# Kernel tuning notes

Hardware: AMD Instinct MI355X
Metric: run time of the kernel (lower is better)

Reference implementation:

```python
import jax, jax.numpy as jnp
import numpy as np

H = 512      # hidden size
V = 10000    # input_output_size (vocab)
L = 32       # max_length
B = 256      # batch
SOS = 1


def setup_inputs() -> dict:
    key = jax.random.key(0)
    ks = jax.random.split(key, 20)
    g = lambda k, shape: jax.random.normal(k, shape, dtype=jnp.float32) * 0.05
    return dict(
        input_tensor=jax.random.randint(ks[0], (B, L), 0, V),
        target_tensor=jax.random.randint(ks[1], (B, L), 0, V),
        # encoder: embedding + GRU
        enc_embed=g(ks[2], (V, H)),
        enc_w_ih=g(ks[3], (3 * H, H)), enc_w_hh=g(ks[4], (3 * H, H)),
        enc_b_ih=g(ks[5], (3 * H,)), enc_b_hh=g(ks[6], (3 * H,)),
        # attention decoder: embedding + attn + attn_combine + GRU + out
        dec_embed=g(ks[7], (V, H)),
        attn_w=g(ks[8], (L, 2 * H)), attn_b=g(ks[9], (L,)),
        comb_w=g(ks[10], (H, 2 * H)), comb_b=g(ks[11], (H,)),
        dec_w_ih=g(ks[12], (3 * H, H)), dec_w_hh=g(ks[13], (3 * H, H)),
        dec_b_ih=g(ks[14], (3 * H,)), dec_b_hh=g(ks[15], (3 * H,)),
        out_w=g(ks[16], (V, H)), out_b=g(ks[17], (V,)),
    )


def _gru_step(x, h, w_ih, w_hh, b_ih, b_hh):
    # PyTorch GRUCell math. x, h: [B, H]
    gi = x @ w_ih.T + b_ih          # [B, 3H]
    gh = h @ w_hh.T + b_hh          # [B, 3H]
    i_r, i_z, i_n = jnp.split(gi, 3, axis=-1)
    h_r, h_z, h_n = jnp.split(gh, 3, axis=-1)
    r = jax.nn.sigmoid(i_r + h_r)
    z = jax.nn.sigmoid(i_z + h_z)
    n = jnp.tanh(i_n + r * h_n)
    return (1.0 - z) * n + z * h


def reference(input_tensor, target_tensor,
              enc_embed, enc_w_ih, enc_w_hh, enc_b_ih, enc_b_hh,
              dec_embed, attn_w, attn_b, comb_w, comb_b,
              dec_w_ih, dec_w_hh, dec_b_ih, dec_b_hh, out_w, out_b):
    inp_t = input_tensor.T   # [L, B]
    tgt_t = target_tensor.T  # [L, B]
    h0 = jnp.zeros((B, H), dtype=enc_embed.dtype)

    # ---- encoder: scan over time ----
    def enc_step(h, tok):
        x = enc_embed[tok]  # [B, H]
        h2 = _gru_step(x, h, enc_w_ih, enc_w_hh, enc_b_ih, enc_b_hh)
        return h2, h2       # encoder output == hidden

    enc_hidden, enc_outs = jax.lax.scan(enc_step, h0, inp_t)  # enc_outs: [L, B, H]

    # ---- decoder with teacher forcing (phase='train', ratio=1.0) ----
    sos = jnp.full((1, B), SOS, dtype=tgt_t.dtype)
    dec_inputs = jnp.concatenate([sos, tgt_t[:-1]], axis=0)  # [L, B]

    def dec_step(h, tok):
        emb = dec_embed[tok]                                   # [B, H]
        aw = jax.nn.softmax(jnp.concatenate([emb, h], axis=-1) @ attn_w.T + attn_b)  # [B, L]
        applied = jnp.einsum('bl,lbh->bh', aw, enc_outs)       # attention over encoder outputs
        x = jax.nn.relu(jnp.concatenate([emb, applied], axis=-1) @ comb_w.T + comb_b)
        h2 = _gru_step(x, h, dec_w_ih, dec_w_hh, dec_b_ih, dec_b_hh)
        logits = jax.nn.log_softmax(h2 @ out_w.T + out_b)      # [B, V]
        return h2, logits

    _, network_outputs = jax.lax.scan(dec_step, enc_hidden, dec_inputs)  # [L, B, V]
    return network_outputs
```

## Files before the change

kernel.cpp:

```cpp
#include <hip/hip_runtime.h>

#define HD 512
#define VOC 10000
#define SL 32
#define BA 256
#define BH (BA*HD)

typedef __bf16 b16x8 __attribute__((ext_vector_type(8)));
typedef float f32x4 __attribute__((ext_vector_type(4)));
typedef unsigned u32x4 __attribute__((ext_vector_type(4)));

__device__ __forceinline__ ushort f2bf(float x) {
  unsigned u = __float_as_uint(x);
  u += 0x7fffu + ((u >> 16) & 1u);
  return (ushort)(u >> 16);
}

__device__ __forceinline__ void stg_sc(void* p, u32x4 v) {
  asm volatile("global_store_dwordx4 %0, %1, off sc0 sc1"
               :: "v"(p), "v"(v) : "memory");
}
__device__ __forceinline__ void stg_sc1(void* p, unsigned v) {
  asm volatile("global_store_dword %0, %1, off sc0 sc1"
               :: "v"(p), "v"(v) : "memory");
}
__device__ __forceinline__ void stg_plain(void* p, unsigned v) {
  asm volatile("global_store_dword %0, %1, off"
               :: "v"(p), "v"(v) : "memory");
}
__device__ __forceinline__ unsigned ldg_sc0(const void* p) {
  unsigned v;
  asm volatile("global_load_dword %0, %1, off sc0"
               : "=v"(v) : "v"(p) : "memory");
  asm volatile("s_waitcnt vmcnt(0)" ::: "memory");
  return v;
}
__device__ __forceinline__ unsigned ldg_sc1(const void* p) {
  unsigned v;
  asm volatile("global_load_dword %0, %1, off sc0 sc1"
               : "=v"(v) : "v"(p) : "memory");
  asm volatile("s_waitcnt vmcnt(0)" ::: "memory");
  return v;
}
__device__ __forceinline__ void vmwait0() {
  asm volatile("s_waitcnt vmcnt(0)" ::: "memory");
  __builtin_amdgcn_sched_barrier(0);
}

__global__ __launch_bounds__(256) void cvt3_k(
    const float* __restrict__ w_out, ushort* __restrict__ o_out,
    const float* __restrict__ w_comb, ushort* __restrict__ o_comb,
    const float* __restrict__ w_attn, ushort* __restrict__ o_attn) {
  int b = blockIdx.x;
  const float* in; ushort* out; int i; int n4;
  if (b < 5000)      { in = w_out;  out = o_out;  i = b * 256 + threadIdx.x;          n4 = 1280000; }
  else if (b < 5512) { in = w_comb; out = o_comb; i = (b - 5000) * 256 + threadIdx.x; n4 = 131072; }
  else               { in = w_attn; out = o_attn; i = (b - 5512) * 256 + threadIdx.x; n4 = 8192; }
  if (i < n4) {
    float4 v = ((const float4*)in)[i];
    ((ushort4*)out)[i] = make_ushort4(f2bf(v.x), f2bf(v.y), f2bf(v.z), f2bf(v.w));
  }
}

__global__ __launch_bounds__(64) void gather2_k(
    const float* __restrict__ enc_t, const float* __restrict__ dec_t,
    const int* __restrict__ in_tok, const int* __restrict__ tgt_tok,
    ushort* __restrict__ enc_o, ushort* __restrict__ dec_o) {
  int bid = blockIdx.x;
  int isDec = bid >= SL * BA;
  int row = isDec ? bid - SL * BA : bid;
  int l = row >> 8, b = row & 255;
  int tok = isDec ? ((l == 0) ? 1 : tgt_tok[b * SL + l - 1]) : in_tok[b * SL + l];
  const float* table = isDec ? dec_t : enc_t;
  ushort* out = isDec ? dec_o : enc_o;
  const float4* src = (const float4*)(table + (size_t)tok * HD);
  int t = threadIdx.x;
  float4 v0 = src[t * 2], v1 = src[t * 2 + 1];
  uint4 o;
  o.x = (unsigned)f2bf(v0.x) | ((unsigned)f2bf(v0.y) << 16);
  o.y = (unsigned)f2bf(v0.z) | ((unsigned)f2bf(v0.w) << 16);
  o.z = (unsigned)f2bf(v1.x) | ((unsigned)f2bf(v1.y) << 16);
  o.w = (unsigned)f2bf(v1.z) | ((unsigned)f2bf(v1.w) << 16);
  *(uint4*)(out + (size_t)row * HD + t * 8) = o;
}

__global__ __launch_bounds__(256) void gemm2_k(
    const ushort* __restrict__ A,
    const ushort* __restrict__ Wc, const ushort* __restrict__ Wa,
    const float* __restrict__ bc, const float* __restrict__ ba,
    float* __restrict__ outc, float* __restrict__ outa) {
  __shared__ ushort lsA[4][64][8];
  __shared__ ushort lsB[4][64][8];
  __shared__ float ctile[64][68];
  int t = threadIdx.x;
  int lane = t & 63, w = t >> 6;
  int by = blockIdx.y;
  const ushort* W; const float* bias; float* outf; int N, n0, ldc;
  if (by < 8) { W = Wc; bias = bc; outf = outc; N = 512; n0 = by * 64; ldc = 512; }
  else        { W = Wa; bias = ba; outf = outa; N = 32;  n0 = 0;       ldc = 32; }
  int m0 = blockIdx.x * 64;
  f32x4 acc[4] = {};
  int sr = t >> 2, g = t & 3;
  const ushort* Ap = A + (size_t)(m0 + sr) * HD + g * 8;
  int nr = n0 + sr; if (nr > N - 1) nr = N - 1;
  const ushort* Wp = W + (size_t)nr * 1024 + g * 8;
  for (int ks = 0; ks < 16; ++ks) {
    *(uint4*)(&lsA[g][sr][0]) = *(const uint4*)(Ap + ks * 32);
    *(uint4*)(&lsB[g][sr][0]) = *(const uint4*)(Wp + ks * 32);
    __syncthreads();
    int gg = lane >> 4, r = lane & 15;
    b16x8 bf = *(const b16x8*)(&lsB[gg][w * 16 + r][0]);
#pragma unroll
    for (int mi = 0; mi < 4; ++mi) {
      b16x8 af = *(const b16x8*)(&lsA[gg][mi * 16 + r][0]);
      acc[mi] = __builtin_amdgcn_mfma_f32_16x16x32_bf16(af, bf, acc[mi], 0, 0, 0);
    }
    __syncthreads();
  }
  int gg = lane >> 4, cl = lane & 15;
  int tcol = w * 16 + cl;
  int bc2 = n0 + tcol; if (bc2 > N - 1) bc2 = N - 1;
  float bv = bias[bc2];
#pragma unroll
  for (int mi = 0; mi < 4; ++mi)
#pragma unroll
    for (int r = 0; r < 4; ++r)
      ctile[mi * 16 + gg * 4 + r][tcol] = acc[mi][r] + bv;
  __syncthreads();
  int row = t >> 2, q = t & 3;
#pragma unroll
  for (int j = 0; j < 4; ++j) {
    int c = q * 16 + j * 4;
    if (n0 + c + 3 <= N - 1)
      *(float4*)(outf + (size_t)(m0 + row) * ldc + n0 + c) =
          *(const float4*)&ctile[row][c];
  }
}

__global__ __launch_bounds__(256) void gemmW_k(
    const ushort* __restrict__ A, const ushort* __restrict__ W,
    ushort* __restrict__ outI) {
  __shared__ ushort lsA[4][64][8];
  __shared__ ushort lsB[4][64][8];
  __shared__ ushort ctileS[64][64];
  int t = threadIdx.x, lane = t & 63, w = t >> 6;
  int m0 = blockIdx.x * 64, n0 = blockIdx.y * 64;
  f32x4 acc[4] = {};
  int sr = t >> 2, g = t & 3;
  const ushort* Ap = A + (size_t)(m0 + sr) * HD + g * 8;
  const ushort* Wp = W + (size_t)(n0 + sr) * 1024 + 512 + g * 8;
  for (int ks = 0; ks < 16; ++ks) {
    *(uint4*)(&lsA[g][sr][0]) = *(const uint4*)(Ap + ks * 32);
    *(uint4*)(&lsB[g][sr][0]) = *(const uint4*)(Wp + ks * 32);
    __syncthreads();
    int gg = lane >> 4, r = lane & 15;
    b16x8 bf = *(const b16x8*)(&lsB[gg][w * 16 + r][0]);
#pragma unroll
    for (int mi = 0; mi < 4; ++mi) {
      b16x8 af = *(const b16x8*)(&lsA[gg][mi * 16 + r][0]);
      acc[mi] = __builtin_amdgcn_mfma_f32_16x16x32_bf16(af, bf, acc[mi], 0, 0, 0);
    }
    __syncthreads();
  }
  int gg = lane >> 4, cl = lane & 15;
  int tcol = w * 16 + cl;
#pragma unroll
  for (int mi = 0; mi < 4; ++mi)
#pragma unroll
    for (int r = 0; r < 4; ++r)
      ctileS[mi * 16 + gg * 4 + r][tcol] = f2bf(acc[mi][r]);
  __syncthreads();
  int l = m0 >> 8, b0 = m0 & 255;
  int sl_i = t >> 6, tid = t & 63;
  int sl_g = (n0 >> 4) + sl_i;
  ushort* dst = outI + ((((size_t)sl_g * 256 + b0 + tid) * 32) + l) * 16;
  *(uint4*)dst = *(const uint4*)&ctileS[tid][sl_i * 16];
  *(uint4*)(dst + 8) = *(const uint4*)&ctileS[tid][sl_i * 16 + 8];
}

__global__ __launch_bounds__(256) void gemm128_k(
    const ushort* __restrict__ A, const ushort* __restrict__ W,
    int N, const float* __restrict__ bias,
    float* __restrict__ outf, int ldc) {
  __shared__ ushort lsA[4][128][8];
  __shared__ ushort lsB[4][64][8];
  __shared__ float ctile[128][68];
  int t = threadIdx.x, lane = t & 63, w = t >> 6;
  int m0 = blockIdx.x * 128, n0 = blockIdx.y * 64;
  f32x4 acc[8] = {};
  int arow = t >> 1, ag = t & 1;
  const ushort* Ap = A + (size_t)(m0 + arow) * HD + ag * 16;
  int brow = t >> 2, bg = t & 3;
  int nr = n0 + brow; if (nr > N - 1) nr = N - 1;
  const ushort* Wp = W + (size_t)nr * HD + bg * 8;
  for (int ks = 0; ks < 16; ++ks) {
    *(uint4*)(&lsA[ag * 2][arow][0])     = *(const uint4*)(Ap + ks * 32);
    *(uint4*)(&lsA[ag * 2 + 1][arow][0]) = *(const uint4*)(Ap + ks * 32 + 8);
    *(uint4*)(&lsB[bg][brow][0])         = *(const uint4*)(Wp + ks * 32);
    __syncthreads();
    int gg = lane >> 4, r = lane & 15;
    b16x8 bf = *(const b16x8*)(&lsB[gg][w * 16 + r][0]);
#pragma unroll
    for (int mi = 0; mi < 8; ++mi) {
      b16x8 af = *(const b16x8*)(&lsA[gg][mi * 16 + r][0]);
      acc[mi] = __builtin_amdgcn_mfma_f32_16x16x32_bf16(af, bf, acc[mi], 0, 0, 0);
    }
    __syncthreads();
  }
  int gg = lane >> 4, cl = lane & 15;
  int tcol = w * 16 + cl;
  int bc = n0 + tcol; if (bc > N - 1) bc = N - 1;
  float bv = bias[bc];
#pragma unroll
  for (int mi = 0; mi < 8; ++mi)
#pragma unroll
    for (int r = 0; r < 4; ++r)
      ctile[mi * 16 + gg * 4 + r][tcol] = acc[mi][r] + bv;
  __syncthreads();
  int row = t >> 1, hf = t & 1;
#pragma unroll
  for (int j = 0; j < 8; ++j) {
    int c = hf * 32 + j * 4;
    if (n0 + c + 3 <= N - 1)
      *(float4*)(outf + (size_t)(m0 + row) * ldc + n0 + c) =
          *(const float4*)&ctile[row][c];
  }
}


__device__ __forceinline__ const ushort* sfrag(const ushort* base, int kh,
                                               int gg, int row) {
  return base + (kh * 16 + (gg >> 1)) * 4096 + row * 16 + (gg & 1) * 8;
}

struct EncArgs {
  const ushort* enc_emb_bf;
  const float* enc_w_ih; const float* enc_w_hh;
  const float* enc_b_ih; const float* enc_b_hh;
  ushort* enc_outs_s;
  ushort* enc_outs_rm;
  float* Hc;
  unsigned* fL2; unsigned* fLLC;
};

struct DecArgs {
  const float* dec_w_ih; const float* dec_w_hh;
  const float* dec_b_ih; const float* dec_b_hh;
  const ushort* attn_w_bf;
  const float* attn_pre;
  const float* comb_pre;
  const ushort* enc_outs_s;
  const ushort* encW;
  const float* Hc;
  ushort* H2_s; ushort* H2_rm; ushort* x_s;
  unsigned* fL2; unsigned* fLLC;
};

union DScr {
  float red[2][6][64][4];
  struct { float sS[2][32][33]; float sAW[32][33]; } at;
};

#define BAR_DEFS(fL2p, fLLCp)                                           \
  auto produce = [&](unsigned val) {                                    \
    __syncthreads();                                                    \
    if (w == 0) {                                                       \
      vmwait0();                                                        \
      if (lane == 0) {                                                  \
        stg_plain(&(fL2p)[sl * 4], val);                                \
        stg_sc1(&(fLLCp)[sl * 16], val);                                \
      }                                                                 \
    }                                                                   \
  };                                                                    \
  auto await = [&](unsigned val) {                                      \
    if (w == 0) {                                                       \
      int it = 0;                                                       \
      for (;;) {                                                        \
        unsigned v = ldg_sc0(&(fL2p)[(lane & 31) * 4]);                 \
        if (!__any(v < val)) break;                                     \
        if ((++it & 3) == 0) {                                          \
          unsigned v2 = ldg_sc1(&(fLLCp)[(lane & 31) * 16]);            \
          if (!__any(v < val && v2 < val)) break;                       \
        }                                                               \
        __builtin_amdgcn_s_sleep(1);                                    \
      }                                                                 \
    }                                                                   \
    __syncthreads();                                                    \
  }

#define LOAD_GRU_W32(Wih, Whh)                                          \
  for (int c = w; c < 96; c += 4) {                                     \
    int g = c >> 4, rem = c & 15, kh2 = rem >> 3, ks = rem & 7;         \
    const float* src = (g < 3) ? (Wih) : (Whh);                         \
    int gr = (g % 3) * 512 + sl * 16 + (lane & 15);                     \
    int col = kh2 * 256 + ks * 32 + (lane >> 4) * 8;                    \
    const float4* s4 = (const float4*)(src + (size_t)gr * HD + col);    \
    float4 va = s4[0], vb = s4[1];                                      \
    uint4 o;                                                            \
    o.x = (unsigned)f2bf(va.x) | ((unsigned)f2bf(va.y) << 16);          \
    o.y = (unsigned)f2bf(va.z) | ((unsigned)f2bf(va.w) << 16);          \
    o.z = (unsigned)f2bf(vb.x) | ((unsigned)f2bf(vb.y) << 16);          \
    o.w = (unsigned)f2bf(vb.z) | ((unsigned)f2bf(vb.w) << 16);          \
    *(uint4*)&Wlds[g][kh2][ks][lane][0] = o;                            \
  }

#define GRU_TAIL(b_ih_, b_hh_, hbf_dst_, hrm_dst_)                      \
  if (kh == 1) {                                                        \
    _Pragma("unroll")                                                   \
    for (int s = 0; s < 6; ++s) *(f32x4*)&redp[mf][s][lane][0] = acc[s];\
  }                                                                     \
  __syncthreads();                                                      \
  if (kh == 0) {                                                        \
    int j = sl * 16 + lr;                                               \
    _Pragma("unroll")                                                   \
    for (int s = 0; s < 6; ++s) acc[s] += *(const f32x4*)&redp[mf][s][lane][0]; \
    float bir = (b_ih_)[j], biz = (b_ih_)[512 + j], bin_ = (b_ih_)[1024 + j]; \
    float bhr = (b_hh_)[j], bhz = (b_hh_)[512 + j], bhn = (b_hh_)[1024 + j]; \
    _Pragma("unroll")                                                   \
    for (int ri = 0; ri < 4; ++ri) {                                    \
      float ir = acc[0][ri] + bir, iz = acc[1][ri] + biz, inn = acc[2][ri] + bin_; \
      float hr2 = acc[3][ri] + bhr, hz = acc[4][ri] + bhz, hn = acc[5][ri] + bhn; \
      float rrg = 1.f / (1.f + expf(-(ir + hr2)));                      \
      float zz = 1.f / (1.f + expf(-(iz + hz)));                        \
      float nn = tanhf(inn + rrg * hn);                                 \
      float h2 = (1.f - zz) * nn + zz * hp[ri];                         \
      hp[ri] = h2;                                                      \
      stile[mf * 16 + gg * 4 + ri][lr] = f2bf(h2);                      \
    }                                                                   \
  }                                                                     \
  __syncthreads();                                                      \
  if (t < 64) {                                                         \
    stg_sc((hbf_dst_) + sl * 4096 + r0 * 16 + t * 8, ((const u32x4*)stile)[t]); \
    if (hrm_dst_) {                                                     \
      int row2 = t >> 1, c2 = t & 1;                                    \
      *(uint4*)((hrm_dst_) + (size_t)(r0 + row2) * HD + sl * 16 + c2 * 8) = \
          *(const uint4*)&stile[row2][c2 * 8];                          \
    }                                                                   \
  }

__global__ __launch_bounds__(256) void enc_k(EncArgs a) {
  __shared__ ushort Wlds[6][2][8][64][8];
  __shared__ float red[2][6][64][4];
  __shared__ ushort stile[32][16];
  float (*redp)[6][64][4] = red;
  int bid = blockIdx.x;
  int rg = bid & 7, sl = bid >> 3;
  int t = threadIdx.x, lane = t & 63, w = t >> 6;
  int r0 = rg * 32;
  unsigned* fL2 = a.fL2 + rg * 32 * 4;
  unsigned* fLLC = a.fLLC + rg * 32 * 16;
  BAR_DEFS(fL2, fLLC);

  LOAD_GRU_W32(a.enc_w_ih, a.enc_w_hh);
  __syncthreads();

  int mf = w & 1, kh = w >> 1;
  int lr = lane & 15, gg = lane >> 4;
  int row_a = r0 + mf * 16 + lr;
  float hp[4] = {0.f, 0.f, 0.f, 0.f};

  for (int l = 0; l < SL; ++l) {
    const ushort* xr = a.enc_emb_bf + (size_t)l * BH + (size_t)row_a * HD +
                       kh * 256 + gg * 8;
    b16x8 xa[8];
#pragma unroll
    for (int ks = 0; ks < 8; ++ks) xa[ks] = *(const b16x8*)(xr + ks * 32);
    f32x4 acc[6] = {};
#pragma unroll
    for (int ks = 0; ks < 8; ++ks)
#pragma unroll
      for (int g3 = 0; g3 < 3; ++g3)
        acc[g3] = __builtin_amdgcn_mfma_f32_16x16x32_bf16(
            xa[ks], *(const b16x8*)(&Wlds[g3][kh][ks][lane][0]), acc[g3], 0, 0, 0);
    if (l) await((unsigned)l);
    b16x8 ha[8];
    if (l) {
      const ushort* hr = sfrag(a.enc_outs_s + (size_t)(l - 1) * BH, kh, gg, row_a);
#pragma unroll
      for (int ks = 0; ks < 8; ++ks) ha[ks] = *(const b16x8*)(hr + ks * 8192);
    } else {
#pragma unroll
      for (int ks = 0; ks < 8; ++ks) ha[ks] = b16x8{};
    }
#pragma unroll
    for (int ks = 0; ks < 8; ++ks)
#pragma unroll
      for (int g3 = 0; g3 < 3; ++g3)
        acc[3 + g3] = __builtin_amdgcn_mfma_f32_16x16x32_bf16(
            ha[ks], *(const b16x8*)(&Wlds[3 + g3][kh][ks][lane][0]),
            acc[3 + g3], 0, 0, 0);
    GRU_TAIL(a.enc_b_ih, a.enc_b_hh, a.enc_outs_s + (size_t)l * BH,
             a.enc_outs_rm + (size_t)l * BH);
    if (l != SL - 1) produce((unsigned)(l + 1));
  }
  if ((w >> 1) == 0) {
    int j = sl * 16 + lr;
#pragma unroll
    for (int ri = 0; ri < 4; ++ri)
      a.Hc[(size_t)(r0 + mf * 16 + gg * 4 + ri) * HD + j] = hp[ri];
  }
}

__global__ __launch_bounds__(256) void dec_k(DecArgs a) {
  __shared__ ushort Wlds[6][2][8][64][8];
  __shared__ DScr scr;
  __shared__ ushort stile[32][16];
  float (*redp)[6][64][4] = scr.red;
  int bid = blockIdx.x;
  int rg = bid & 7, sl = bid >> 3;
  int t = threadIdx.x, lane = t & 63, w = t >> 6;
  int r0 = rg * 32;
  unsigned* fL2 = a.fL2 + rg * 32 * 4;
  unsigned* fLLC = a.fLLC + rg * 32 * 16;
  BAR_DEFS(fL2, fLLC);

  LOAD_GRU_W32(a.dec_w_ih, a.dec_w_hh);

  int mf = w & 1, kh = w >> 1;
  int lr = lane & 15, gg = lane >> 4;
  int row_a = r0 + mf * 16 + lr;
  int rr = t >> 3, dp = t & 7;

  float hp[4] = {0.f, 0.f, 0.f, 0.f};
  if ((w >> 1) == 0) {
    int j = sl * 16 + lr;
#pragma unroll
    for (int ri = 0; ri < 4; ++ri)
      hp[ri] = a.Hc[(size_t)(r0 + mf * 16 + gg * 4 + ri) * HD + j];
  }
  __syncthreads();

  for (int l = 0; l < SL; ++l) {
    const ushort* h_bf = l ? a.H2_s + (size_t)(l - 1) * BH
                           : a.enc_outs_s + (size_t)31 * BH;
    unsigned ev[32];
    {
      const ushort* ep = a.encW + (((size_t)sl * 256 + r0 + rr) * 32) * 16 + dp * 2;
#pragma unroll
      for (int ll = 0; ll < 32; ++ll)
        ev[ll] = *(const unsigned*)(ep + ll * 16);
    }
    if (l) await(2u * l);
    {
      const ushort* hr = sfrag(h_bf, kh, gg, row_a);
      const ushort* w0 = a.attn_w_bf + (size_t)lr * 1024 + 512 + kh * 256 + gg * 8;
      const ushort* w1 = a.attn_w_bf + (size_t)(16 + lr) * 1024 + 512 + kh * 256 + gg * 8;
      f32x4 a0 = {}, a1 = {};
#pragma unroll
      for (int ks = 0; ks < 8; ++ks) {
        b16x8 ah = *(const b16x8*)(hr + ks * 8192);
        a0 = __builtin_amdgcn_mfma_f32_16x16x32_bf16(
            ah, *(const b16x8*)(w0 + ks * 32), a0, 0, 0, 0);
        a1 = __builtin_amdgcn_mfma_f32_16x16x32_bf16(
            ah, *(const b16x8*)(w1 + ks * 32), a1, 0, 0, 0);
      }
#pragma unroll
      for (int ri = 0; ri < 4; ++ri) {
        scr.at.sS[kh][mf * 16 + gg * 4 + ri][lr] = a0[ri];
        scr.at.sS[kh][mf * 16 + gg * 4 + ri][16 + lr] = a1[ri];
      }
    }
    __syncthreads();
    {
      float4 pre = *(const float4*)(a.attn_pre + ((size_t)l * BA + r0 + rr) * 32 + dp * 4);
      float v0 = scr.at.sS[0][rr][dp * 4 + 0] + scr.at.sS[1][rr][dp * 4 + 0] + pre.x;
      float v1 = scr.at.sS[0][rr][dp * 4 + 1] + scr.at.sS[1][rr][dp * 4 + 1] + pre.y;
      float v2 = scr.at.sS[0][rr][dp * 4 + 2] + scr.at.sS[1][rr][dp * 4 + 2] + pre.z;
      float v3 = scr.at.sS[0][rr][dp * 4 + 3] + scr.at.sS[1][rr][dp * 4 + 3] + pre.w;
      float mx = fmaxf(fmaxf(v0, v1), fmaxf(v2, v3));
      for (int o = 1; o < 8; o <<= 1) mx = fmaxf(mx, __shfl_xor(mx, o, 64));
      float e0 = expf(v0 - mx), e1 = expf(v1 - mx);
      float e2 = expf(v2 - mx), e3 = expf(v3 - mx);
      float s = e0 + e1 + e2 + e3;
      for (int o = 1; o < 8; o <<= 1) s += __shfl_xor(s, o, 64);
      float inv = 1.f / s;
      scr.at.sAW[rr][dp * 4 + 0] = e0 * inv; scr.at.sAW[rr][dp * 4 + 1] = e1 * inv;
      scr.at.sAW[rr][dp * 4 + 2] = e2 * inv; scr.at.sAW[rr][dp * 4 + 3] = e3 * inv;
    }
    __syncthreads();
    {
      const float* cp = a.comb_pre + ((size_t)l * BA + r0 + rr) * HD + sl * 16 + dp * 2;
      float f0 = cp[0], f1 = cp[1];
#pragma unroll
      for (int ll = 0; ll < 32; ++ll) {
        float aw = scr.at.sAW[rr][ll];
        f0 += aw * __uint_as_float(ev[ll] << 16);
        f1 += aw * __uint_as_float(ev[ll] & 0xffff0000u);
      }
      f0 = fmaxf(f0, 0.f); f1 = fmaxf(f1, 0.f);
      *(unsigned*)&stile[rr][dp * 2] =
          (unsigned)f2bf(f0) | ((unsigned)f2bf(f1) << 16);
    }
    __syncthreads();
    if (t < 64)
      stg_sc(a.x_s + (size_t)l * BH + sl * 4096 + r0 * 16 + t * 8,
             ((const u32x4*)stile)[t]);
    produce(2u * l + 1);
    f32x4 acc[6] = {};
    {
      const ushort* hr = sfrag(h_bf, kh, gg, row_a);
      b16x8 ha[8];
#pragma unroll
      for (int ks = 0; ks < 8; ++ks) ha[ks] = *(const b16x8*)(hr + ks * 8192);
#pragma unroll
      for (int ks = 0; ks < 8; ++ks)
#pragma unroll
        for (int g3 = 0; g3 < 3; ++g3)
          acc[3 + g3] = __builtin_amdgcn_mfma_f32_16x16x32_bf16(
              ha[ks], *(const b16x8*)(&Wlds[3 + g3][kh][ks][lane][0]),
              acc[3 + g3], 0, 0, 0);
    }
    await(2u * l + 1);
    {
      const ushort* xr = sfrag(a.x_s + (size_t)l * BH, kh, gg, row_a);
      b16x8 xa[8];
#pragma unroll
      for (int ks = 0; ks < 8; ++ks) xa[ks] = *(const b16x8*)(xr + ks * 8192);
#pragma unroll
      for (int ks = 0; ks < 8; ++ks)
#pragma unroll
        for (int g3 = 0; g3 < 3; ++g3)
          acc[g3] = __builtin_amdgcn_mfma_f32_16x16x32_bf16(
              xa[ks], *(const b16x8*)(&Wlds[g3][kh][ks][lane][0]),
              acc[g3], 0, 0, 0);
    }
    GRU_TAIL(a.dec_b_ih, a.dec_b_hh, a.H2_s + (size_t)l * BH,
             a.H2_rm + (size_t)l * BH);
    if (l != SL - 1) produce(2u * l + 2);
  }
}

__global__ __launch_bounds__(256) void lsesub_k(float* __restrict__ logits) {
  __shared__ float redm[4], reds[4];
  int row = blockIdx.x, t = threadIdx.x;
  float4* p = (float4*)(logits + (size_t)row * VOC);
  float4 v[10];
  float m = -1e30f, s = 0.f;
#pragma unroll
  for (int j = 0; j < 10; ++j) {
    int i = t + j * 256;
    if (i < 2500) {
      v[j] = p[i];
      float mx = fmaxf(fmaxf(v[j].x, v[j].y), fmaxf(v[j].z, v[j].w));
      if (mx > m) { s *= expf(m - mx); m = mx; }
      s += expf(v[j].x - m) + expf(v[j].y - m) + expf(v[j].z - m) + expf(v[j].w - m);
    }
  }
#pragma unroll
  for (int o = 32; o; o >>= 1) {
    float m2 = __shfl_xor(m, o, 64), s2 = __shfl_xor(s, o, 64);
    float mn = fmaxf(m, m2);
    s = s * expf(m - mn) + s2 * expf(m2 - mn);
    m = mn;
  }
  if ((t & 63) == 0) { redm[t >> 6] = m; reds[t >> 6] = s; }
  __syncthreads();
  float mf = fmaxf(fmaxf(redm[0], redm[1]), fmaxf(redm[2], redm[3]));
  float sf = reds[0] * expf(redm[0] - mf) + reds[1] * expf(redm[1] - mf) +
             reds[2] * expf(redm[2] - mf) + reds[3] * expf(redm[3] - mf);
  float z = mf + logf(sf);
#pragma unroll
  for (int j = 0; j < 10; ++j) {
    int i = t + j * 256;
    if (i < 2500) {
      v[j].x -= z; v[j].y -= z; v[j].z -= z; v[j].w -= z;
      p[i] = v[j];
    }
  }
}

extern "C" void kernel_launch(void* const* d_in, const int* in_sizes, int n_in,
                              void* d_out, int out_size, void* d_ws, size_t ws_size,
                              hipStream_t stream) {
  (void)in_sizes; (void)n_in; (void)out_size; (void)ws_size;
  const int* in_tok = (const int*)d_in[0];
  const int* tgt_tok = (const int*)d_in[1];
  const float* enc_embed = (const float*)d_in[2];
  const float* enc_w_ih = (const float*)d_in[3];
  const float* enc_w_hh = (const float*)d_in[4];
  const float* enc_b_ih = (const float*)d_in[5];
  const float* enc_b_hh = (const float*)d_in[6];
  const float* dec_embed = (const float*)d_in[7];
  const float* attn_w = (const float*)d_in[8];
  const float* attn_b = (const float*)d_in[9];
  const float* comb_w = (const float*)d_in[10];
  const float* comb_b = (const float*)d_in[11];
  const float* dec_w_ih = (const float*)d_in[12];
  const float* dec_w_hh = (const float*)d_in[13];
  const float* dec_b_ih = (const float*)d_in[14];
  const float* dec_b_hh = (const float*)d_in[15];
  const float* out_w = (const float*)d_in[16];
  const float* out_b = (const float*)d_in[17];
  float* out = (float*)d_out;

  char* ws = (char*)d_ws;
  size_t off = 0;
  auto carve = [&](size_t bytes) {
    void* p = ws + off;
    off += (bytes + 255) & ~(size_t)255;
    return p;
  };
  ushort* comb_w_bf  = (ushort*)carve(512 * 1024 * 2);
  ushort* attn_w_bf  = (ushort*)carve(32 * 1024 * 2);
  ushort* out_w_bf   = (ushort*)carve((size_t)VOC * HD * 2);
  ushort* enc_emb_bf = (ushort*)carve((size_t)SL * BA * HD * 2);
  ushort* dec_emb_bf = (ushort*)carve((size_t)SL * BA * HD * 2);
  float* attn_pre    = (float*)carve((size_t)SL * BA * 32 * 4);
  float* comb_pre    = (float*)carve((size_t)SL * BA * HD * 4);
  ushort* enc_outs_s = (ushort*)carve((size_t)SL * BA * HD * 2);
  ushort* enc_outs_rm= (ushort*)carve((size_t)SL * BA * HD * 2);
  ushort* encW       = (ushort*)carve((size_t)SL * BA * HD * 2);
  ushort* H2_s       = (ushort*)carve((size_t)SL * BA * HD * 2);
  ushort* H2_rm      = (ushort*)carve((size_t)SL * BA * HD * 2);
  ushort* x_s        = (ushort*)carve((size_t)SL * BA * HD * 2);
  float* Hc          = (float*)carve((size_t)BA * HD * 4);
  unsigned* fE_L2    = (unsigned*)carve(8 * 32 * 4 * 4);
  unsigned* fE_LLC   = (unsigned*)carve(8 * 32 * 16 * 4);
  unsigned* fD_L2    = (unsigned*)carve(8 * 32 * 4 * 4);
  unsigned* fD_LLC   = (unsigned*)carve(8 * 32 * 16 * 4);

  hipMemsetAsync(fE_L2, 0, (8 * 32 * 4 + 8 * 32 * 16) * 2 * 4, stream);
  cvt3_k<<<5544, 256, 0, stream>>>(out_w, out_w_bf, comb_w, comb_w_bf,
                                   attn_w, attn_w_bf);
  gather2_k<<<2 * SL * BA, 64, 0, stream>>>(enc_embed, dec_embed, in_tok,
                                            tgt_tok, enc_emb_bf, dec_emb_bf);

  gemm2_k<<<dim3(128, 9), 256, 0, stream>>>(dec_emb_bf, comb_w_bf, attn_w_bf,
                                            comb_b, attn_b, comb_pre, attn_pre);

  EncArgs ea;
  ea.enc_emb_bf = enc_emb_bf;
  ea.enc_w_ih = enc_w_ih; ea.enc_w_hh = enc_w_hh;
  ea.enc_b_ih = enc_b_ih; ea.enc_b_hh = enc_b_hh;
  ea.enc_outs_s = enc_outs_s;
  ea.enc_outs_rm = enc_outs_rm;
  ea.Hc = Hc;
  ea.fL2 = fE_L2; ea.fLLC = fE_LLC;
  void* ekargs[] = { (void*)&ea };
  hipError_t ce = hipLaunchCooperativeKernel(enc_k, dim3(256), dim3(256),
                                             ekargs, 0, stream);
  if (ce != hipSuccess) enc_k<<<256, 256, 0, stream>>>(ea);

  gemmW_k<<<dim3(128, 8), 256, 0, stream>>>(enc_outs_rm, comb_w_bf, encW);

  DecArgs da;
  da.dec_w_ih = dec_w_ih; da.dec_w_hh = dec_w_hh;
  da.dec_b_ih = dec_b_ih; da.dec_b_hh = dec_b_hh;
  da.attn_w_bf = attn_w_bf;
  da.attn_pre = attn_pre;
  da.comb_pre = comb_pre;
  da.enc_outs_s = enc_outs_s;
  da.encW = encW;
  da.Hc = Hc;
  da.H2_s = H2_s; da.H2_rm = H2_rm; da.x_s = x_s;
  da.fL2 = fD_L2; da.fLLC = fD_LLC;
  void* dkargs[] = { (void*)&da };
  ce = hipLaunchCooperativeKernel(dec_k, dim3(256), dim3(256),
                                  dkargs, 0, stream);
  if (ce != hipSuccess) dec_k<<<256, 256, 0, stream>>>(da);

  gemm128_k<<<dim3(64, 157), 256, 0, stream>>>(H2_rm, out_w_bf, VOC,
                                               out_b, out, VOC);
  lsesub_k<<<SL * BA, 256, 0, stream>>>(out);
}
```

Baseline: 856.5 us.

## Halve recurrent kernel grid, simplify flag barrier, widen output GEMM tile

Result: slower. 1.183 ms (+38.1%).

```diff
diff --git a/kernel.cpp b/kernel.cpp
--- a/kernel.cpp
+++ b/kernel.cpp
@@ -23,17 +23,6 @@
 __device__ __forceinline__ void stg_sc1(void* p, unsigned v) {
   asm volatile("global_store_dword %0, %1, off sc0 sc1"
                :: "v"(p), "v"(v) : "memory");
-}
-__device__ __forceinline__ void stg_plain(void* p, unsigned v) {
-  asm volatile("global_store_dword %0, %1, off"
-               :: "v"(p), "v"(v) : "memory");
-}
-__device__ __forceinline__ unsigned ldg_sc0(const void* p) {
-  unsigned v;
-  asm volatile("global_load_dword %0, %1, off sc0"
-               : "=v"(v) : "v"(p) : "memory");
-  asm volatile("s_waitcnt vmcnt(0)" ::: "memory");
-  return v;
 }
 __device__ __forceinline__ unsigned ldg_sc1(const void* p) {
   unsigned v;
@@ -178,52 +167,63 @@
   *(uint4*)(dst + 8) = *(const uint4*)&ctileS[tid][sl_i * 16 + 8];
 }
 
-__global__ __launch_bounds__(256) void gemm128_k(
+__global__ __launch_bounds__(256) void gemmbig_k(
     const ushort* __restrict__ A, const ushort* __restrict__ W,
     int N, const float* __restrict__ bias,
     float* __restrict__ outf, int ldc) {
   __shared__ ushort lsA[4][128][8];
-  __shared__ ushort lsB[4][64][8];
-  __shared__ float ctile[128][68];
+  __shared__ ushort lsB[4][128][8];
+  __shared__ float ctile[64][132];
   int t = threadIdx.x, lane = t & 63, w = t >> 6;
-  int m0 = blockIdx.x * 128, n0 = blockIdx.y * 64;
-  f32x4 acc[8] = {};
+  int m0 = blockIdx.x * 128, n0 = blockIdx.y * 128;
+  f32x4 acc[8][2] = {};
   int arow = t >> 1, ag = t & 1;
   const ushort* Ap = A + (size_t)(m0 + arow) * HD + ag * 16;
-  int brow = t >> 2, bg = t & 3;
-  int nr = n0 + brow; if (nr > N - 1) nr = N - 1;
-  const ushort* Wp = W + (size_t)nr * HD + bg * 8;
+  int nr = n0 + arow; if (nr > N - 1) nr = N - 1;
+  const ushort* Wp = W + (size_t)nr * HD + ag * 16;
   for (int ks = 0; ks < 16; ++ks) {
     *(uint4*)(&lsA[ag * 2][arow][0])     = *(const uint4*)(Ap + ks * 32);
     *(uint4*)(&lsA[ag * 2 + 1][arow][0]) = *(const uint4*)(Ap + ks * 32 + 8);
-    *(uint4*)(&lsB[bg][brow][0])         = *(const uint4*)(Wp + ks * 32);
+    *(uint4*)(&lsB[ag * 2][arow][0])     = *(const uint4*)(Wp + ks * 32);
+    *(uint4*)(&lsB[ag * 2 + 1][arow][0]) = *(const uint4*)(Wp + ks * 32 + 8);
     __syncthreads();
     int gg = lane >> 4, r = lane & 15;
-    b16x8 bf = *(const b16x8*)(&lsB[gg][w * 16 + r][0]);
+    b16x8 bf0 = *(const b16x8*)(&lsB[gg][w * 32 + r][0]);
+    b16x8 bf1 = *(const b16x8*)(&lsB[gg][w * 32 + 16 + r][0]);
 #pragma unroll
     for (int mi = 0; mi < 8; ++mi) {
       b16x8 af = *(const b16x8*)(&lsA[gg][mi * 16 + r][0]);
-      acc[mi] = __builtin_amdgcn_mfma_f32_16x16x32_bf16(af, bf, acc[mi], 0, 0, 0);
+      acc[mi][0] = __builtin_amdgcn_mfma_f32_16x16x32_bf16(af, bf0, acc[mi][0], 0, 0, 0);
+      acc[mi][1] = __builtin_amdgcn_mfma_f32_16x16x32_bf16(af, bf1, acc[mi][1], 0, 0, 0);
     }
     __syncthreads();
   }
   int gg = lane >> 4, cl = lane & 15;
-  int tcol = w * 16 + cl;
-  int bc = n0 + tcol; if (bc > N - 1) bc = N - 1;
-  float bv = bias[bc];
-#pragma unroll
-  for (int mi = 0; mi < 8; ++mi)
-#pragma unroll
-    for (int r = 0; r < 4; ++r)
-      ctile[mi * 16 + gg * 4 + r][tcol] = acc[mi][r] + bv;
-  __syncthreads();
-  int row = t >> 1, hf = t & 1;
-#pragma unroll
-  for (int j = 0; j < 8; ++j) {
-    int c = hf * 32 + j * 4;
-    if (n0 + c + 3 <= N - 1)
-      *(float4*)(outf + (size_t)(m0 + row) * ldc + n0 + c) =
-          *(const float4*)&ctile[row][c];
+#pragma unroll
+  for (int half = 0; half < 2; ++half) {
+    __syncthreads();
+#pragma unroll
+    for (int mi = 0; mi < 4; ++mi) {
+      int m = half * 4 + mi;
+#pragma unroll
+      for (int nf = 0; nf < 2; ++nf) {
+        int tc = w * 32 + nf * 16 + cl;
+        int bc = n0 + tc; if (bc > N - 1) bc = N - 1;
+        float bv = bias[bc];
+#pragma unroll
+        for (int r2 = 0; r2 < 4; ++r2)
+          ctile[mi * 16 + gg * 4 + r2][tc] = acc[m][nf][r2] + bv;
+      }
+    }
+    __syncthreads();
+    int row = t >> 2, q = t & 3;
+#pragma unroll
+    for (int j = 0; j < 8; ++j) {
+      int c = q * 32 + j * 4;
+      if (n0 + c + 3 <= N - 1)
+        *(float4*)(outf + (size_t)(m0 + half * 64 + row) * ldc + n0 + c) =
+            *(const float4*)&ctile[row][c];
+    }
   }
 }
 
@@ -240,7 +240,7 @@
   ushort* enc_outs_s;
   ushort* enc_outs_rm;
   float* Hc;
-  unsigned* fL2; unsigned* fLLC;
+  unsigned* fLLC;
 };
 
 struct DecArgs {
@@ -253,7 +253,7 @@
   const ushort* encW;
   const float* Hc;
   ushort* H2_s; ushort* H2_rm; ushort* x_s;
-  unsigned* fL2; unsigned* fLLC;
+  unsigned* fLLC;
 };
 
 union DScr {
@@ -261,27 +261,19 @@
   struct { float sS[2][32][33]; float sAW[32][33]; } at;
 };
 
-#define BAR_DEFS(fL2p, fLLCp)                                           \
-  auto produce = [&](unsigned val) {                                    \
+#define BAR_DEFS(fFp)                                                   \
+  auto produce = [&](int rg, unsigned val) {                            \
     __syncthreads();                                                    \
     if (w == 0) {                                                       \
       vmwait0();                                                        \
-      if (lane == 0) {                                                  \
-        stg_plain(&(fL2p)[sl * 4], val);                                \
-        stg_sc1(&(fLLCp)[sl * 16], val);                                \
-      }                                                                 \
+      if (lane == 0) stg_sc1(&(fFp)[rg * 512 + sl * 16], val);          \
     }                                                                   \
   };                                                                    \
-  auto await = [&](unsigned val) {                                      \
+  auto await = [&](int rg, unsigned val) {                              \
     if (w == 0) {                                                       \
-      int it = 0;                                                       \
       for (;;) {                                                        \
-        unsigned v = ldg_sc0(&(fL2p)[(lane & 31) * 4]);                 \
+        unsigned v = ldg_sc1(&(fFp)[rg * 512 + (lane & 31) * 16]);      \
         if (!__any(v < val)) break;                                     \
-        if ((++it & 3) == 0) {                                          \
-          unsigned v2 = ldg_sc1(&(fLLCp)[(lane & 31) * 16]);            \
-          if (!__any(v < val && v2 < val)) break;                       \
-        }                                                               \
         __builtin_amdgcn_s_sleep(1);                                    \
       }                                                                 \
     }                                                                   \
@@ -304,7 +296,7 @@
     *(uint4*)&Wlds[g][kh2][ks][lane][0] = o;                            \
   }
 
-#define GRU_TAIL(b_ih_, b_hh_, hbf_dst_, hrm_dst_)                      \
+#define GRU_TAIL(hpA, b_ih_, b_hh_, hbf_dst_, hrm_dst_)                 \
   if (kh == 1) {                                                        \
     _Pragma("unroll")                                                   \
     for (int s = 0; s < 6; ++s) *(f32x4*)&redp[mf][s][lane][0] = acc[s];\
@@ -323,19 +315,17 @@
       float rrg = 1.f / (1.f + expf(-(ir + hr2)));                      \
       float zz = 1.f / (1.f + expf(-(iz + hz)));                        \
       float nn = tanhf(inn + rrg * hn);                                 \
-      float h2 = (1.f - zz) * nn + zz * hp[ri];                         \
-      hp[ri] = h2;                                                      \
+      float h2 = (1.f - zz) * nn + zz * (hpA)[ri];                      \
+      (hpA)[ri] = h2;                                                   \
       stile[mf * 16 + gg * 4 + ri][lr] = f2bf(h2);                      \
     }                                                                   \
   }                                                                     \
   __syncthreads();                                                      \
   if (t < 64) {                                                         \
     stg_sc((hbf_dst_) + sl * 4096 + r0 * 16 + t * 8, ((const u32x4*)stile)[t]); \
-    if (hrm_dst_) {                                                     \
-      int row2 = t >> 1, c2 = t & 1;                                    \
-      *(uint4*)((hrm_dst_) + (size_t)(r0 + row2) * HD + sl * 16 + c2 * 8) = \
-          *(const uint4*)&stile[row2][c2 * 8];                          \
-    }                                                                   \
+    int row2 = t >> 1, c2 = t & 1;                                      \
+    *(uint4*)((hrm_dst_) + (size_t)(r0 + row2) * HD + sl * 16 + c2 * 8) = \
+        *(const uint4*)&stile[row2][c2 * 8];                            \
   }
 
 __global__ __launch_bounds__(256) void enc_k(EncArgs a) {
@@ -344,60 +334,65 @@
   __shared__ ushort stile[32][16];
   float (*redp)[6][64][4] = red;
   int bid = blockIdx.x;
-  int rg = bid & 7, sl = bid >> 3;
+  int rp = bid & 3, sl = bid >> 2;
   int t = threadIdx.x, lane = t & 63, w = t >> 6;
-  int r0 = rg * 32;
-  unsigned* fL2 = a.fL2 + rg * 32 * 4;
-  unsigned* fLLC = a.fLLC + rg * 32 * 16;
-  BAR_DEFS(fL2, fLLC);
+  BAR_DEFS(a.fLLC);
 
   LOAD_GRU_W32(a.enc_w_ih, a.enc_w_hh);
   __syncthreads();
 
   int mf = w & 1, kh = w >> 1;
   int lr = lane & 15, gg = lane >> 4;
-  int row_a = r0 + mf * 16 + lr;
-  float hp[4] = {0.f, 0.f, 0.f, 0.f};
+  float hp[2][4] = {};
 
   for (int l = 0; l < SL; ++l) {
-    const ushort* xr = a.enc_emb_bf + (size_t)l * BH + (size_t)row_a * HD +
-                       kh * 256 + gg * 8;
-    b16x8 xa[8];
-#pragma unroll
-    for (int ks = 0; ks < 8; ++ks) xa[ks] = *(const b16x8*)(xr + ks * 32);
-    f32x4 acc[6] = {};
-#pragma unroll
-    for (int ks = 0; ks < 8; ++ks)
-#pragma unroll
-      for (int g3 = 0; g3 < 3; ++g3)
-        acc[g3] = __builtin_amdgcn_mfma_f32_16x16x32_bf16(
-            xa[ks], *(const b16x8*)(&Wlds[g3][kh][ks][lane][0]), acc[g3], 0, 0, 0);
-    if (l) await((unsigned)l);
-    b16x8 ha[8];
-    if (l) {
-      const ushort* hr = sfrag(a.enc_outs_s + (size_t)(l - 1) * BH, kh, gg, row_a);
-#pragma unroll
-      for (int ks = 0; ks < 8; ++ks) ha[ks] = *(const b16x8*)(hr + ks * 8192);
-    } else {
-#pragma unroll
-      for (int ks = 0; ks < 8; ++ks) ha[ks] = b16x8{};
-    }
-#pragma unroll
-    for (int ks = 0; ks < 8; ++ks)
-#pragma unroll
-      for (int g3 = 0; g3 < 3; ++g3)
-        acc[3 + g3] = __builtin_amdgcn_mfma_f32_16x16x32_bf16(
-            ha[ks], *(const b16x8*)(&Wlds[3 + g3][kh][ks][lane][0]),
-            acc[3 + g3], 0, 0, 0);
-    GRU_TAIL(a.enc_b_ih, a.enc_b_hh, a.enc_outs_s + (size_t)l * BH,
-             a.enc_outs_rm + (size_t)l * BH);
-    if (l != SL - 1) produce((unsigned)(l + 1));
-  }
-  if ((w >> 1) == 0) {
-    int j = sl * 16 + lr;
-#pragma unroll
-    for (int ri = 0; ri < 4; ++ri)
-      a.Hc[(size_t)(r0 + mf * 16 + gg * 4 + ri) * HD + j] = hp[ri];
+#pragma unroll
+    for (int c = 0; c < 2; ++c) {
+      int rg = rp + c * 4, r0 = rg * 32;
+      int row_a = r0 + mf * 16 + lr;
+      const ushort* xr = a.enc_emb_bf + (size_t)l * BH + (size_t)row_a * HD +
+                         kh * 256 + gg * 8;
+      b16x8 xa[8];
+#pragma unroll
+      for (int ks = 0; ks < 8; ++ks) xa[ks] = *(const b16x8*)(xr + ks * 32);
+      f32x4 acc[6] = {};
+#pragma unroll
+      for (int ks = 0; ks < 8; ++ks)
+#pragma unroll
+        for (int g3 = 0; g3 < 3; ++g3)
+          acc[g3] = __builtin_amdgcn_mfma_f32_16x16x32_bf16(
+              xa[ks], *(const b16x8*)(&Wlds[g3][kh][ks][lane][0]), acc[g3], 0, 0, 0);
+      if (l) await(rg, (unsigned)l);
+      b16x8 ha[8];
+      if (l) {
+        const ushort* hr = sfrag(a.enc_outs_s + (size_t)(l - 1) * BH, kh, gg, row_a);
+#pragma unroll
+        for (int ks = 0; ks < 8; ++ks) ha[ks] = *(const b16x8*)(hr + ks * 8192);
+      } else {
+#pragma unroll
+        for (int ks = 0; ks < 8; ++ks) ha[ks] = b16x8{};
+      }
+#pragma unroll
+      for (int ks = 0; ks < 8; ++ks)
+#pragma unroll
+        for (int g3 = 0; g3 < 3; ++g3)
+          acc[3 + g3] = __builtin_amdgcn_mfma_f32_16x16x32_bf16(
+              ha[ks], *(const b16x8*)(&Wlds[3 + g3][kh][ks][lane][0]),
+              acc[3 + g3], 0, 0, 0);
+      GRU_TAIL(hp[c], a.enc_b_ih, a.enc_b_hh, a.enc_outs_s + (size_t)l * BH,
+               a.enc_outs_rm + (size_t)l * BH);
+      if (l != SL - 1) produce(rg, (unsigned)(l + 1));
+    }
+  }
+  if (kh == 0) {
+#pragma unroll
+    for (int c = 0; c < 2; ++c) {
+      int r0 = (rp + c * 4) * 32;
+      int j = sl * 16 + lr;
+#pragma unroll
+      for (int ri = 0; ri < 4; ++ri)
+        a.Hc[(size_t)(r0 + mf * 16 + gg * 4 + ri) * HD + j] = hp[c][ri];
+    }
   }
 }
 
@@ -407,126 +402,133 @@
   __shared__ ushort stile[32][16];
   float (*redp)[6][64][4] = scr.red;
   int bid = blockIdx.x;
-  int rg = bid & 7, sl = bid >> 3;
+  int rp = bid & 3, sl = bid >> 2;
   int t = threadIdx.x, lane = t & 63, w = t >> 6;
-  int r0 = rg * 32;
-  unsigned* fL2 = a.fL2 + rg * 32 * 4;
-  unsigned* fLLC = a.fLLC + rg * 32 * 16;
-  BAR_DEFS(fL2, fLLC);
+  BAR_DEFS(a.fLLC);
 
   LOAD_GRU_W32(a.dec_w_ih, a.dec_w_hh);
 
   int mf = w & 1, kh = w >> 1;
   int lr = lane & 15, gg = lane >> 4;
-  int row_a = r0 + mf * 16 + lr;
   int rr = t >> 3, dp = t & 7;
 
-  float hp[4] = {0.f, 0.f, 0.f, 0.f};
-  if ((w >> 1) == 0) {
-    int j = sl * 16 + lr;
-#pragma unroll
-    for (int ri = 0; ri < 4; ++ri)
-      hp[ri] = a.Hc[(size_t)(r0 + mf * 16 + gg * 4 + ri) * HD + j];
+  float hp[2][4] = {};
+  if (kh == 0) {
+#pragma unroll
+    for (int c = 0; c < 2; ++c) {
+      int r0 = (rp + c * 4) * 32;
+      int j = sl * 16 + lr;
+#pragma unroll
+      for (int ri = 0; ri < 4; ++ri)
+        hp[c][ri] = a.Hc[(size_t)(r0 + mf * 16 + gg * 4 + ri) * HD + j];
+    }
   }
   __syncthreads();
 
   for (int l = 0; l < SL; ++l) {
     const ushort* h_bf = l ? a.H2_s + (size_t)(l - 1) * BH
                            : a.enc_outs_s + (size_t)31 * BH;
-    unsigned ev[32];
-    {
+#pragma unroll
+    for (int c = 0; c < 2; ++c) {
+      int rg = rp + c * 4, r0 = rg * 32;
+      int row_a = r0 + mf * 16 + lr;
+      unsigned ev[32];
       const ushort* ep = a.encW + (((size_t)sl * 256 + r0 + rr) * 32) * 16 + dp * 2;
 #pragma unroll
-      for (int ll = 0; ll < 32; ++ll)
-        ev[ll] = *(const unsigned*)(ep + ll * 16);
-    }
-    if (l) await(2u * l);
-    {
-      const ushort* hr = sfrag(h_bf, kh, gg, row_a);
-      const ushort* w0 = a.attn_w_bf + (size_t)lr * 1024 + 512 + kh * 256 + gg * 8;
-      const ushort* w1 = a.attn_w_bf + (size_t)(16 + lr) * 1024 + 512 + kh * 256 + gg * 8;
-      f32x4 a0 = {}, a1 = {};
-#pragma unroll
-      for (int ks = 0; ks < 8; ++ks) {
-        b16x8 ah = *(const b16x8*)(hr + ks * 8192);
-        a0 = __builtin_amdgcn_mfma_f32_16x16x32_bf16(
-            ah, *(const b16x8*)(w0 + ks * 32), a0, 0, 0, 0);
-        a1 = __builtin_amdgcn_mfma_f32_16x16x32_bf16(
-            ah, *(const b16x8*)(w1 + ks * 32), a1, 0, 0, 0);
+      for (int ll = 0; ll < 32; ++ll) ev[ll] = *(const unsigned*)(ep + ll * 16);
+      if (l) await(rg, 2u * l);
+      {
+        const ushort* hr = sfrag(h_bf, kh, gg, row_a);
+        const ushort* w0p = a.attn_w_bf + (size_t)lr * 1024 + 512 + kh * 256 + gg * 8;
+        const ushort* w1p = a.attn_w_bf + (size_t)(16 + lr) * 1024 + 512 + kh * 256 + gg * 8;
+        f32x4 a0 = {}, a1 = {};
+#pragma unroll
+        for (int ks = 0; ks < 8; ++ks) {
+          b16x8 ah = *(const b16x8*)(hr + ks * 8192);
+          a0 = __builtin_amdgcn_mfma_f32_16x16x32_bf16(
+              ah, *(const b16x8*)(w0p + ks * 32), a0, 0, 0, 0);
+          a1 = __builtin_amdgcn_mfma_f32_16x16x32_bf16(
+              ah, *(const b16x8*)(w1p + ks * 32), a1, 0, 0, 0);
+        }
+#pragma unroll
+        for (int ri = 0; ri < 4; ++ri) {
+          scr.at.sS[kh][mf * 16 + gg * 4 + ri][lr] = a0[ri];
+          scr.at.sS[kh][mf * 16 + gg * 4 + ri][16 + lr] = a1[ri];
+        }
       }
-#pragma unroll
-      for (int ri = 0; ri < 4; ++ri) {
-        scr.at.sS[kh][mf * 16 + gg * 4 + ri][lr] = a0[ri];
-        scr.at.sS[kh][mf * 16 + gg * 4 + ri][16 + lr] = a1[ri];
+      __syncthreads();
+      {
+        float4 pre = *(const float4*)(a.attn_pre + ((size_t)l * BA + r0 + rr) * 32 + dp * 4);
+        float v0 = scr.at.sS[0][rr][dp * 4 + 0] + scr.at.sS[1][rr][dp * 4 + 0] + pre.x;
+        float v1 = scr.at.sS[0][rr][dp * 4 + 1] + scr.at.sS[1][rr][dp * 4 + 1] + pre.y;
+        float v2 = scr.at.sS[0][rr][dp * 4 + 2] + scr.at.sS[1][rr][dp * 4 + 2] + pre.z;
+        float v3 = scr.at.sS[0][rr][dp * 4 + 3] + scr.at.sS[1][rr][dp * 4 + 3] + pre.w;
+        float mx = fmaxf(fmaxf(v0, v1), fmaxf(v2, v3));
+        for (int o = 1; o < 8; o <<= 1) mx = fmaxf(mx, __shfl_xor(mx, o, 64));
+        float e0 = expf(v0 - mx), e1 = expf(v1 - mx);
+        float e2 = expf(v2 - mx), e3 = expf(v3 - mx);
+        float s = e0 + e1 + e2 + e3;
+        for (int o = 1; o < 8; o <<= 1) s += __shfl_xor(s, o, 64);
+        float inv = 1.f / s;
+        scr.at.sAW[rr][dp * 4 + 0] = e0 * inv; scr.at.sAW[rr][dp * 4 + 1] = e1 * inv;
+        scr.at.sAW[rr][dp * 4 + 2] = e2 * inv; scr.at.sAW[rr][dp * 4 + 3] = e3 * inv;
       }
-    }
-    __syncthreads();
-    {
-      float4 pre = *(const float4*)(a.attn_pre + ((size_t)l * BA + r0 + rr) * 32 + dp * 4);
-      float v0 = scr.at.sS[0][rr][dp * 4 + 0] + scr.at.sS[1][rr][dp * 4 + 0] + pre.x;
-      float v1 = scr.at.sS[0][rr][dp * 4 + 1] + scr.at.sS[1][rr][dp * 4 + 1] + pre.y;
-      float v2 = scr.at.sS[0][rr][dp * 4 + 2] + scr.at.sS[1][rr][dp * 4 + 2] + pre.z;
-      float v3 = scr.at.sS[0][rr][dp * 4 + 3] + scr.at.sS[1][rr][dp * 4 + 3] + pre.w;
-      float mx = fmaxf(fmaxf(v0, v1), fmaxf(v2, v3));
-      for (int o = 1; o < 8; o <<= 1) mx = fmaxf(mx, __shfl_xor(mx, o, 64));
-      float e0 = expf(v0 - mx), e1 = expf(v1 - mx);
-      float e2 = expf(v2 - mx), e3 = expf(v3 - mx);
-      float s = e0 + e1 + e2 + e3;
-      for (int o = 1; o < 8; o <<= 1) s += __shfl_xor(s, o, 64);
-      float inv = 1.f / s;
-      scr.at.sAW[rr][dp * 4 + 0] = e0 * inv; scr.at.sAW[rr][dp * 4 + 1] = e1 * inv;
-      scr.at.sAW[rr][dp * 4 + 2] = e2 * inv; scr.at.sAW[rr][dp * 4 + 3] = e3 * inv;
-    }
-    __syncthreads();
-    {
-      const float* cp = a.comb_pre + ((size_t)l * BA + r0 + rr) * HD + sl * 16 + dp * 2;
-      float f0 = cp[0], f1 = cp[1];
-#pragma unroll
-      for (int ll = 0; ll < 32; ++ll) {
-        float aw = scr.at.sAW[rr][ll];
-        f0 += aw * __uint_as_float(ev[ll] << 16);
-        f1 += aw * __uint_as_float(ev[ll] & 0xffff0000u);
+      __syncthreads();
+      {
+        const float* cp = a.comb_pre + ((size_t)l * BA + r0 + rr) * HD + sl * 16 + dp * 2;
+        float f0 = cp[0], f1 = cp[1];
+#pragma unroll
+        for (int ll = 0; ll < 32; ++ll) {
+          float aw = scr.at.sAW[rr][ll];
+          f0 += aw * __uint_as_float(ev[ll] << 16);
+          f1 += aw * __uint_as_float(ev[ll] & 0xffff0000u);
+        }
+        f0 = fmaxf(f0, 0.f); f1 = fmaxf(f1, 0.f);
+        *(unsigned*)&stile[rr][dp * 2] =
+            (unsigned)f2bf(f0) | ((unsigned)f2bf(f1) << 16);
       }
-      f0 = fmaxf(f0, 0.f); f1 = fmaxf(f1, 0.f);
-      *(unsigned*)&stile[rr][dp * 2] =
-          (unsigned)f2bf(f0) | ((unsigned)f2bf(f1) << 16);
-    }
-    __syncthreads();
-    if (t < 64)
-      stg_sc(a.x_s + (size_t)l * BH + sl * 4096 + r0 * 16 + t * 8,
-             ((const u32x4*)stile)[t]);
-    produce(2u * l + 1);
-    f32x4 acc[6] = {};
-    {
-      const ushort* hr = sfrag(h_bf, kh, gg, row_a);
-      b16x8 ha[8];
-#pragma unroll
-      for (int ks = 0; ks < 8; ++ks) ha[ks] = *(const b16x8*)(hr + ks * 8192);
-#pragma unroll
-      for (int ks = 0; ks < 8; ++ks)
-#pragma unroll
-        for (int g3 = 0; g3 < 3; ++g3)
-          acc[3 + g3] = __builtin_amdgcn_mfma_f32_16x16x32_bf16(
-              ha[ks], *(const b16x8*)(&Wlds[3 + g3][kh][ks][lane][0]),
-              acc[3 + g3], 0, 0, 0);
-    }
-    await(2u * l + 1);
-    {
-      const ushort* xr = sfrag(a.x_s + (size_t)l * BH, kh, gg, row_a);
-      b16x8 xa[8];
-#pragma unroll
-      for (int ks = 0; ks < 8; ++ks) xa[ks] = *(const b16x8*)(xr + ks * 8192);
-#pragma unroll
-      for (int ks = 0; ks < 8; ++ks)
-#pragma unroll
-        for (int g3 = 0; g3 < 3; ++g3)
-          acc[g3] = __builtin_amdgcn_mfma_f32_16x16x32_bf16(
-              xa[ks], *(const b16x8*)(&Wlds[g3][kh][ks][lane][0]),
-              acc[g3], 0, 0, 0);
-    }
-    GRU_TAIL(a.dec_b_ih, a.dec_b_hh, a.H2_s + (size_t)l * BH,
-             a.H2_rm + (size_t)l * BH);
-    if (l != SL - 1) produce(2u * l + 2);
+      __syncthreads();
+      if (t < 64)
+        stg_sc(a.x_s + (size_t)l * BH + sl * 4096 + r0 * 16 + t * 8,
+               ((const u32x4*)stile)[t]);
+      produce(rg, 2u * l + 1);
+    }
+#pragma unroll
+    for (int c = 0; c < 2; ++c) {
+      int rg = rp + c * 4, r0 = rg * 32;
+      int row_a = r0 + mf * 16 + lr;
+      f32x4 acc[6] = {};
+      {
+        const ushort* hr = sfrag(h_bf, kh, gg, row_a);
+        b16x8 ha[8];
+#pragma unroll
+        for (int ks = 0; ks < 8; ++ks) ha[ks] = *(const b16x8*)(hr + ks * 8192);
+#pragma unroll
+        for (int ks = 0; ks < 8; ++ks)
+#pragma unroll
+          for (int g3 = 0; g3 < 3; ++g3)
+            acc[3 + g3] = __builtin_amdgcn_mfma_f32_16x16x32_bf16(
+                ha[ks], *(const b16x8*)(&Wlds[3 + g3][kh][ks][lane][0]),
+                acc[3 + g3], 0, 0, 0);
+      }
+      await(rg, 2u * l + 1);
+      {
+        const ushort* xr = sfrag(a.x_s + (size_t)l * BH, kh, gg, row_a);
+        b16x8 xa[8];
+#pragma unroll
+        for (int ks = 0; ks < 8; ++ks) xa[ks] = *(const b16x8*)(xr + ks * 8192);
+#pragma unroll
+        for (int ks = 0; ks < 8; ++ks)
+#pragma unroll
+          for (int g3 = 0; g3 < 3; ++g3)
+            acc[g3] = __builtin_amdgcn_mfma_f32_16x16x32_bf16(
+                xa[ks], *(const b16x8*)(&Wlds[g3][kh][ks][lane][0]),
+                acc[g3], 0, 0, 0);
+      }
+      GRU_TAIL(hp[c], a.dec_b_ih, a.dec_b_hh, a.H2_s + (size_t)l * BH,
+               a.H2_rm + (size_t)l * BH);
+      if (l != SL - 1) produce(rg, 2u * l + 2);
+    }
   }
 }
 
@@ -614,12 +616,11 @@
   ushort* H2_rm      = (ushort*)carve((size_t)SL * BA * HD * 2);
   ushort* x_s        = (ushort*)carve((size_t)SL * BA * HD * 2);
   float* Hc          = (float*)carve((size_t)BA * HD * 4);
-  unsigned* fE_L2    = (unsigned*)carve(8 * 32 * 4 * 4);
   unsigned* fE_LLC   = (unsigned*)carve(8 * 32 * 16 * 4);
-  unsigned* fD_L2    = (unsigned*)carve(8 * 32 * 4 * 4);
   unsigned* fD_LLC   = (unsigned*)carve(8 * 32 * 16 * 4);
 
-  hipMemsetAsync(fE_L2, 0, (8 * 32 * 4 + 8 * 32 * 16) * 2 * 4, stream);
+  hipMemsetAsync(fE_LLC, 0, 8 * 32 * 16 * 4, stream);
+  hipMemsetAsync(fD_LLC, 0, 8 * 32 * 16 * 4, stream);
   cvt3_k<<<5544, 256, 0, stream>>>(out_w, out_w_bf, comb_w, comb_w_bf,
                                    attn_w, attn_w_bf);
   gather2_k<<<2 * SL * BA, 64, 0, stream>>>(enc_embed, dec_embed, in_tok,
@@ -635,11 +636,11 @@
   ea.enc_outs_s = enc_outs_s;
   ea.enc_outs_rm = enc_outs_rm;
   ea.Hc = Hc;
-  ea.fL2 = fE_L2; ea.fLLC = fE_LLC;
+  ea.fLLC = fE_LLC;
   void* ekargs[] = { (void*)&ea };
-  hipError_t ce = hipLaunchCooperativeKernel(enc_k, dim3(256), dim3(256),
+  hipError_t ce = hipLaunchCooperativeKernel(enc_k, dim3(128), dim3(256),
                                              ekargs, 0, stream);
-  if (ce != hipSuccess) enc_k<<<256, 256, 0, stream>>>(ea);
+  if (ce != hipSuccess) enc_k<<<128, 256, 0, stream>>>(ea);
 
   gemmW_k<<<dim3(128, 8), 256, 0, stream>>>(enc_outs_rm, comb_w_bf, encW);
 
@@ -653,13 +654,13 @@
   da.encW = encW;
   da.Hc = Hc;
   da.H2_s = H2_s; da.H2_rm = H2_rm; da.x_s = x_s;
-  da.fL2 = fD_L2; da.fLLC = fD_LLC;
+  da.fLLC = fD_LLC;
   void* dkargs[] = { (void*)&da };
-  ce = hipLaunchCooperativeKernel(dec_k, dim3(256), dim3(256),
+  ce = hipLaunchCooperativeKernel(dec_k, dim3(128), dim3(256),
                                   dkargs, 0, stream);
-  if (ce != hipSuccess) dec_k<<<256, 256, 0, stream>>>(da);
-
-  gemm128_k<<<dim3(64, 157), 256, 0, stream>>>(H2_rm, out_w_bf, VOC,
-                                               out_b, out, VOC);
+  if (ce != hipSuccess) dec_k<<<128, 256, 0, stream>>>(da);
+
+  gemmbig_k<<<dim3(64, 79), 256, 0, stream>>>(H2_rm, out_w_bf, VOC,
+                                              out_b, out, VOC);
   lsesub_k<<<SL * BA, 256, 0, stream>>>(out);
 }
```
